# Kernel tuning notes

Hardware: AMD Instinct MI355X
Metric: run time of the kernel (lower is better)

## Reference

```python
import jax, jax.numpy as jnp
import numpy as np
from bisect import bisect

# hyperparameters (from init_kwargs)
DELTA = 1e-4
GAMMA = 0.1
UTILITY_SCALE = -0.01
PRIORITY_RAIL = 0.5
LOSS_BALANCE = 1.0
ALPHA_ELU = 1.0
ENTROPY_THRESHOLDS = [0, 10, 50]
ENTROPY_LEVELS = [0.0, 0.05, 0.1, 1.0]
MASK_LEVEL = 10000.0

N = 512


def setup_inputs() -> dict:
    key = jax.random.key(0)
    k1, k2, k3, k4 = jax.random.split(key, 4)
    soft_adj = jax.random.uniform(k1, (N, N), dtype=jnp.float32)
    # original adjacency is a binary {0,1} float mask
    original_adj = (jax.random.uniform(k2, (N, N)) > 0.5).astype(jnp.float32)
    distances = jax.random.uniform(k3, (N, N), dtype=jnp.float32) * 100.0
    flow = jax.random.uniform(k4, (N, N), dtype=jnp.float32) * 10.0
    epoch = 20  # python int, selects entropy penalty level via bisect
    return {"soft_adj": soft_adj, "original_adj": original_adj,
            "distances": distances, "flow": flow, "epoch": epoch}


def _shortest_path(soft_adj, distances):
    """Soft (softmin via logsumexp) Floyd-Warshall all-pairs shortest path."""
    W = distances / (soft_adj + DELTA)          # [N, N] effective edge weights
    n = W.shape[0]
    w0 = W * (1.0 - jnp.eye(n, dtype=W.dtype))  # zero diagonal

    def step(w, k):
        # softmin(w, w[:,k,None] + w[None,k,:]) without materializing a stack
        path_through_k = w[:, k][:, None] + w[k, :][None, :]
        w_new = -GAMMA * jnp.logaddexp(-w / GAMMA, -path_through_k / GAMMA)
        return w_new, None

    w_dist, _ = jax.lax.scan(step, w0, jnp.arange(n))
    return w_dist


def reference(soft_adj, original_adj, distances, flow, epoch):
    loss_cost = jnp.sum(soft_adj * distances)

    shortest_paths = _shortest_path(soft_adj, distances)

    exp_ut_rail = jnp.exp(UTILITY_SCALE * shortest_paths * PRIORITY_RAIL)
    exp_ut_base = jnp.exp(UTILITY_SCALE * distances)
    choice_matrix = exp_ut_rail / (exp_ut_rail + exp_ut_base)
    distance_saved = distances - PRIORITY_RAIL * shortest_paths
    utility_gain = flow * choice_matrix * distance_saved
    utility_gain = jax.nn.elu(utility_gain, alpha=ALPHA_ELU) + ALPHA_ELU

    inverse_soft = jnp.eye(soft_adj.shape[0], dtype=soft_adj.dtype) - soft_adj
    entropy_loss = jnp.sum(jnp.square(soft_adj * inverse_soft))
    entropy_scale = ENTROPY_LEVELS[bisect(ENTROPY_THRESHOLDS, epoch)]

    mask_loss = jnp.sum(soft_adj * (1.0 - original_adj))

    return (loss_cost
            + LOSS_BALANCE * jnp.sum(utility_gain)
            + entropy_loss * entropy_scale
            + MASK_LEVEL * mask_loss)
```

## Files before the change

kernel.cpp:

```cpp
#include <hip/hip_runtime.h>
#include <math.h>

#define NN 512
#define KP 64
#define NPANEL 8
#define NTHR 256
#define NBLK 256
#define TRUNITS (448 * 112)

#define D_   0
#define V_   4160
#define B2_  8320
#define UB_  12672
#define SB_  17024
#define H_   21376
#define LDSN 25728

__device__ __forceinline__ float einit(const float* s, const float* dI, int i, int j) {
  float w = dI[i * NN + j] / (s[i * NN + j] + 1e-4f);
  if (i == j) w = 0.f;
  return expf(-10.f * w);
}

__global__ __launch_bounds__(NTHR) void fw_phase(
    const float* __restrict__ s, const float* __restrict__ dI,
    float* __restrict__ E, float* __restrict__ Cs, float* __restrict__ Rs,
    float* __restrict__ out, int p) {
  __shared__ __align__(16) float lds[LDSN];
  const int blk = blockIdx.x, tid = threadIdx.x;
  const int k0 = p * KP;

  if (blk >= 32) {
    const int gt = (blk - 32) * NTHR + tid;
    if (p == 0) {
      if (blk == 32 && tid == 0) out[0] = 0.f;
      if (gt < TRUNITS) {
        const int ii = gt / 112;
        const int jj = gt - ii * 112;
        const int i = ii + KP;
        const int j = (jj + 16) << 2;
        const int idx = i * NN + j;
        const float4 sv = *(const float4*)(s + idx);
        const float4 dv = *(const float4*)(dI + idx);
        float w0 = dv.x / (sv.x + 1e-4f); if (i == j + 0) w0 = 0.f;
        float w1 = dv.y / (sv.y + 1e-4f); if (i == j + 1) w1 = 0.f;
        float w2 = dv.z / (sv.z + 1e-4f); if (i == j + 2) w2 = 0.f;
        float w3 = dv.w / (sv.w + 1e-4f); if (i == j + 3) w3 = 0.f;
        *(float4*)(E + idx) = make_float4(expf(-10.f * w0), expf(-10.f * w1),
                                          expf(-10.f * w2), expf(-10.f * w3));
      }
    } else if (gt < TRUNITS) {
      const int ii = gt / 112;
      const int jj = gt - ii * 112;
      const int i = (ii < k0) ? ii : ii + KP;
      const int j = ((jj < (p << 4)) ? jj : jj + 16) << 2;
      const int idx = i * NN + j;
      const float* Cprev = Cs + (size_t)(p - 1) * (NN * KP);
      const float* Rprev = Rs + (size_t)(p - 1) * (KP * NN);
      float4 acc = *(const float4*)(E + idx);
      const float* crow = Cprev + (size_t)i * KP;
      const float* rcol = Rprev + j;
#pragma unroll 8
      for (int r = 0; r < KP; ++r) {
        const float cv = crow[r];
        const float4 rv = *(const float4*)(rcol + (size_t)r * NN);
        acc.x += cv * rv.x; acc.y += cv * rv.y;
        acc.z += cv * rv.z; acc.w += cv * rv.w;
      }
      *(float4*)(E + idx) = acc;
    }
    return;
  }

  const bool isC = (blk < 16);
  const int sb = (blk >> 1) & 7;
  const int h = blk & 1;
  const int sOff = sb * KP;
  const bool haveSl = (sb != p);
  const float* Cprev = Cs + (size_t)(p - 1) * (NN * KP);
  const float* Rprev = Rs + (size_t)(p - 1) * (KP * NN);

  if (p == 0) {
    for (int e = tid; e < 4096; e += NTHR) {
      const int a = e >> 6, b = e & 63;
      const float v = einit(s, dI, a, b);
      lds[D_ + a * 65 + b] = v;
      if (blk == 0) E[a * NN + b] = v;
    }
    if (haveSl) {
      if (isC) {
        for (int e = tid; e < 2048; e += NTHR) {
          const int a = 32 * h + (e >> 6), b = e & 63;
          const float v = einit(s, dI, sOff + a, b);
          lds[V_ + a * 65 + b] = v;
          E[(sOff + a) * NN + b] = v;
        }
      } else {
        for (int e = tid; e < 2048; e += NTHR) {
          const int m = e >> 5, j = 32 * h + (e & 31);
          const float v = einit(s, dI, m, sOff + j);
          lds[V_ + j * 65 + m] = v;
          E[m * NN + (sOff + j)] = v;
        }
      }
    }
  } else {
#pragma unroll
    for (int k = 0; k < 4; ++k) {
      const int e4 = tid + k * NTHR;
      const int a = e4 >> 4, b4 = (e4 & 15) << 2;
      *(float4*)&lds[B2_ + a * 68 + b4] =
          *(const float4*)(Cprev + (size_t)(k0 + a) * KP + b4);
      *(float4*)&lds[UB_ + a * 68 + b4] =
          *(const float4*)(Rprev + (size_t)a * NN + (k0 + b4));
      if (haveSl) {
        if (isC)
          *(float4*)&lds[SB_ + a * 68 + b4] =
              *(const float4*)(Cprev + (size_t)(sOff + a) * KP + b4);
        else
          *(float4*)&lds[SB_ + a * 68 + b4] =
              *(const float4*)(Rprev + (size_t)a * NN + (sOff + b4));
      }
    }
    __syncthreads();
    {
      const int r0 = (tid >> 4) << 2, m0 = (tid & 15) << 2;
      float acc[4][4];
#pragma unroll
      for (int i2 = 0; i2 < 4; ++i2) {
        const float4 ev = *(const float4*)(E + (size_t)(k0 + r0 + i2) * NN + (k0 + m0));
        acc[i2][0] = ev.x; acc[i2][1] = ev.y; acc[i2][2] = ev.z; acc[i2][3] = ev.w;
      }
      for (int rr = 0; rr < KP; ++rr) {
        const float4 b4 = *(const float4*)&lds[UB_ + rr * 68 + m0];
#pragma unroll
        for (int i2 = 0; i2 < 4; ++i2) {
          const float av = lds[B2_ + (r0 + i2) * 68 + rr];
          acc[i2][0] += av * b4.x; acc[i2][1] += av * b4.y;
          acc[i2][2] += av * b4.z; acc[i2][3] += av * b4.w;
        }
      }
#pragma unroll
      for (int i2 = 0; i2 < 4; ++i2)
#pragma unroll
        for (int j2 = 0; j2 < 4; ++j2)
          lds[D_ + (r0 + i2) * 65 + (m0 + j2)] = acc[i2][j2];
    }
  }
  __syncthreads();

  if (tid < 64) {
    float x[64];
    if (isC) {
#pragma unroll
      for (int a = 0; a < 64; ++a) x[a] = lds[D_ + a * 65 + tid];
    } else {
#pragma unroll
      for (int a = 0; a < 64; ++a) x[a] = lds[D_ + tid * 65 + a];
    }
#pragma unroll
    for (int m = 0; m < 64; ++m) {
      const float xm = x[m];
      lds[H_ + m * 68 + tid] = xm;
#pragma unroll
      for (int a = 0; a < 64; ++a) {
        const int sa = __builtin_amdgcn_readlane(__float_as_int(x[a]), m);
        x[a] += __int_as_float(sa) * xm;
      }
    }
  } else if (tid < 192) {
    const int tt = tid - 64;
    if (haveSl && p > 0) {
      float acc[4][4];
      if (isC) {
        const int r0 = 32 * h + ((tt >> 4) << 2);
        const int m0 = (tt & 15) << 2;
#pragma unroll
        for (int i2 = 0; i2 < 4; ++i2) {
          const float4 ev = *(const float4*)(E + (size_t)(sOff + r0 + i2) * NN + (k0 + m0));
          acc[i2][0] = ev.x; acc[i2][1] = ev.y; acc[i2][2] = ev.z; acc[i2][3] = ev.w;
        }
        for (int rr = 0; rr < KP; ++rr) {
          const float4 b4 = *(const float4*)&lds[UB_ + rr * 68 + m0];
#pragma unroll
          for (int i2 = 0; i2 < 4; ++i2) {
            const float av = lds[SB_ + (r0 + i2) * 68 + rr];
            acc[i2][0] += av * b4.x; acc[i2][1] += av * b4.y;
            acc[i2][2] += av * b4.z; acc[i2][3] += av * b4.w;
          }
        }
#pragma unroll
        for (int i2 = 0; i2 < 4; ++i2) {
          *(float4*)(E + (size_t)(sOff + r0 + i2) * NN + (k0 + m0)) =
              make_float4(acc[i2][0], acc[i2][1], acc[i2][2], acc[i2][3]);
#pragma unroll
          for (int j2 = 0; j2 < 4; ++j2)
            lds[V_ + (r0 + i2) * 65 + (m0 + j2)] = acc[i2][j2];
        }
      } else {
        const int r0 = (tt & 15) << 2;
        const int c0 = 32 * h + ((tt >> 4) << 2);
#pragma unroll
        for (int i2 = 0; i2 < 4; ++i2) {
          const float4 ev = *(const float4*)(E + (size_t)(k0 + r0 + i2) * NN + (sOff + c0));
          acc[i2][0] = ev.x; acc[i2][1] = ev.y; acc[i2][2] = ev.z; acc[i2][3] = ev.w;
        }
        for (int rr = 0; rr < KP; ++rr) {
          const float4 b4 = *(const float4*)&lds[SB_ + rr * 68 + c0];
#pragma unroll
          for (int i2 = 0; i2 < 4; ++i2) {
            const float av = lds[B2_ + (r0 + i2) * 68 + rr];
            acc[i2][0] += av * b4.x; acc[i2][1] += av * b4.y;
            acc[i2][2] += av * b4.z; acc[i2][3] += av * b4.w;
          }
        }
#pragma unroll
        for (int i2 = 0; i2 < 4; ++i2) {
          *(float4*)(E + (size_t)(k0 + r0 + i2) * NN + (sOff + c0)) =
              make_float4(acc[i2][0], acc[i2][1], acc[i2][2], acc[i2][3]);
#pragma unroll
          for (int j2 = 0; j2 < 4; ++j2)
            lds[V_ + (c0 + j2) * 65 + (r0 + i2)] = acc[i2][j2];
        }
      }
    } else if (!haveSl) {
      for (int e = tt; e < 4096; e += 128) {
        const int a = e >> 6, b = e & 63;
        lds[V_ + a * 65 + b] = isC ? lds[D_ + a * 65 + b] : lds[D_ + b * 65 + a];
      }
    }
  }
  __syncthreads();

  for (int cch = 0; cch < 4; ++cch) {
    const int mb = cch * 16;
    if (cch > 0 && tid < 128) {
      const int r = 32 * h + (tid & 31);
      const int g = tid >> 5;
      const int m0c = mb + 4 * g;
      const int vb = V_ + r * 65;
      float a0 = lds[vb + m0c + 0], a1 = lds[vb + m0c + 1];
      float a2 = lds[vb + m0c + 2], a3 = lds[vb + m0c + 3];
      for (int mp = 0; mp < mb; ++mp) {
        const float vr = lds[vb + mp];
        const float4 u4 = *(const float4*)&lds[H_ + mp * 68 + m0c];
        a0 += vr * u4.x; a1 += vr * u4.y; a2 += vr * u4.z; a3 += vr * u4.w;
      }
      lds[vb + m0c + 0] = a0; lds[vb + m0c + 1] = a1;
      lds[vb + m0c + 2] = a2; lds[vb + m0c + 3] = a3;
    }
    __syncthreads();
    if (tid < 32) {
      const int r = 32 * h + tid;
      const int vb = V_ + r * 65 + mb;
      float v[16];
#pragma unroll
      for (int u2 = 0; u2 < 16; ++u2) v[u2] = lds[vb + u2];
#pragma unroll
      for (int mp = 0; mp < 15; ++mp) {
        const float vmp = v[mp];
#pragma unroll
        for (int m2 = mp + 1; m2 < 16; ++m2)
          v[m2] += vmp * lds[H_ + (mb + mp) * 68 + (mb + m2)];
      }
#pragma unroll
      for (int u2 = 0; u2 < 16; ++u2) lds[vb + u2] = v[u2];
    }
    __syncthreads();
  }

  float* Cp = Cs + (size_t)p * (NN * KP);
  float* Rp = Rs + (size_t)p * (KP * NN);
  if (isC) {
    for (int e = tid; e < 2048; e += NTHR) {
      const int a = 32 * h + (e >> 6), b = e & 63;
      Cp[(size_t)(sOff + a) * KP + b] = lds[V_ + a * 65 + b];
    }
  } else {
    for (int e = tid; e < 2048; e += NTHR) {
      const int m = e >> 5, j = 32 * h + (e & 31);
      Rp[(size_t)m * NN + (sOff + j)] = lds[V_ + j * 65 + m];
    }
  }
}

__device__ __forceinline__ float loss_elem(float Ev, float sv, float ov,
                                           float dv, float fv, int i, int j,
                                           float esc) {
  const float sp = (Ev > 0.f) ? (-0.1f * logf(Ev)) : 1e9f;
  const float ur = expf(-0.005f * sp);
  const float ub = expf(-0.01f * dv);
  const float choice = ur / (ur + ub);
  const float ug = fv * choice * (dv - 0.5f * sp);
  const float util = (ug > 0.f) ? (ug + 1.f) : expf(ug);
  const float ent = sv * (((i == j) ? 1.f : 0.f) - sv);
  return sv * dv + util + esc * ent * ent + 10000.f * (sv * (1.f - ov));
}

__global__ __launch_bounds__(NTHR) void k_loss(
    const float* __restrict__ s, const float* __restrict__ o,
    const float* __restrict__ dI, const float* __restrict__ f,
    const int* __restrict__ ep, const float* __restrict__ E,
    const float* __restrict__ Cs, const float* __restrict__ Rs,
    float* __restrict__ out) {
  __shared__ float red[NTHR];
  const int tid = threadIdx.x;
  const int g = blockIdx.x * NTHR + tid;
  const int idx0 = g * 4;
  const int i = idx0 >> 9;
  const int j = idx0 & (NN - 1);
  const float* C7 = Cs + (size_t)7 * (NN * KP);
  const float* R7 = Rs + (size_t)7 * (KP * NN);
  float4 acc = *(const float4*)(E + idx0);
  {
    const float* crow = C7 + (size_t)i * KP;
    const float* rcol = R7 + j;
#pragma unroll 8
    for (int r = 0; r < KP; ++r) {
      const float cv = crow[r];
      const float4 rv = *(const float4*)(rcol + (size_t)r * NN);
      acc.x += cv * rv.x; acc.y += cv * rv.y;
      acc.z += cv * rv.z; acc.w += cv * rv.w;
    }
  }
  const int bi = i >> 6, bj = j >> 6;
  if (bi == bj && bi >= 1) {
    const float* cf = Cs + (size_t)(bi - 1) * (NN * KP) + (size_t)i * KP;
    const float* rf = Rs + (size_t)(bi - 1) * (KP * NN) + j;
#pragma unroll 8
    for (int r = 0; r < KP; ++r) {
      const float cv = cf[r];
      const float4 rv = *(const float4*)(rf + (size_t)r * NN);
      acc.x += cv * rv.x; acc.y += cv * rv.y;
      acc.z += cv * rv.z; acc.w += cv * rv.w;
    }
  }
  const float4 sv = *(const float4*)(s + idx0);
  const float4 ov = *(const float4*)(o + idx0);
  const float4 dv = *(const float4*)(dI + idx0);
  const float4 fv = *(const float4*)(f + idx0);
  const int e = ep[0];
  const float esc = (e < 0) ? 0.f : (e < 10) ? 0.05f : (e < 50) ? 0.1f : 1.f;
  float lsum = loss_elem(acc.x, sv.x, ov.x, dv.x, fv.x, i, j + 0, esc)
             + loss_elem(acc.y, sv.y, ov.y, dv.y, fv.y, i, j + 1, esc)
             + loss_elem(acc.z, sv.z, ov.z, dv.z, fv.z, i, j + 2, esc)
             + loss_elem(acc.w, sv.w, ov.w, dv.w, fv.w, i, j + 3, esc);
  red[tid] = lsum;
  __syncthreads();
#pragma unroll
  for (int st = 128; st > 0; st >>= 1) {
    if (tid < st) red[tid] += red[tid + st];
    __syncthreads();
  }
  if (tid == 0) atomicAdd(out, red[0]);
}

extern "C" void kernel_launch(void* const* d_in, const int* in_sizes, int n_in,
                              void* d_out, int out_size, void* d_ws, size_t ws_size,
                              hipStream_t stream) {
  const float* s = (const float*)d_in[0];
  const float* o = (const float*)d_in[1];
  const float* d = (const float*)d_in[2];
  const float* f = (const float*)d_in[3];
  const int* ep = (const int*)d_in[4];

  float* E = (float*)d_ws;
  float* Cs = E + NN * NN;
  float* Rs = Cs + NPANEL * NN * KP;
  float* out = (float*)d_out;

  for (int p = 0; p < NPANEL; ++p)
    fw_phase<<<NBLK, NTHR, 0, stream>>>(s, d, E, Cs, Rs, out, p);
  k_loss<<<NBLK, NTHR, 0, stream>>>(s, o, d, f, ep, E, Cs, Rs, out);
}
```

Baseline: 244.5 us.

## Split panel-0 into a small kernel and fuse E initialization into phase one

Panel 0's pivot and panel factorization now run in a dedicated 32-block kernel that writes only the C and R panels. The initial exp-weight matrix is no longer materialized in E during phase 0; phase 1 computes those values on the fly from s and d wherever it would have read E. The diagonal block for phase 1 is written separately by otherwise idle threads. This removes a full pass of writing and re-reading E plus the wide phase-0 launch, at the cost of recomputing divisions and exps inside phase 1 and more branching.

```diff
diff --git a/kernel.cpp b/kernel.cpp
--- a/kernel.cpp
+++ b/kernel.cpp
@@ -22,53 +22,153 @@
   return expf(-10.f * w);
 }
 
+__global__ __launch_bounds__(NTHR) void fw_p0(
+    const float* __restrict__ s, const float* __restrict__ dI,
+    float* __restrict__ Cs, float* __restrict__ Rs, float* __restrict__ out) {
+  __shared__ __align__(16) float lds[LDSN];
+  const int blk = blockIdx.x, tid = threadIdx.x;
+  const bool isC = (blk < 16);
+  const int sb = (blk >> 1) & 7;
+  const int h = blk & 1;
+  const int sOff = sb * KP;
+  const bool haveSl = (sb != 0);
+  if (blk == 0 && tid == 0) out[0] = 0.f;
+
+  for (int e = tid; e < 4096; e += NTHR) {
+    const int a = e >> 6, b = e & 63;
+    lds[D_ + a * 65 + b] = einit(s, dI, a, b);
+  }
+  if (haveSl) {
+    if (isC) {
+      for (int e = tid; e < 2048; e += NTHR) {
+        const int a = 32 * h + (e >> 6), b = e & 63;
+        lds[V_ + a * 65 + b] = einit(s, dI, sOff + a, b);
+      }
+    } else {
+      for (int e = tid; e < 2048; e += NTHR) {
+        const int m = e >> 5, j = 32 * h + (e & 31);
+        lds[V_ + j * 65 + m] = einit(s, dI, m, sOff + j);
+      }
+    }
+  }
+  __syncthreads();
+
+  if (tid < 64) {
+    float x[64];
+    if (isC) {
+#pragma unroll
+      for (int a = 0; a < 64; ++a) x[a] = lds[D_ + a * 65 + tid];
+    } else {
+#pragma unroll
+      for (int a = 0; a < 64; ++a) x[a] = lds[D_ + tid * 65 + a];
+    }
+#pragma unroll
+    for (int m = 0; m < 64; ++m) {
+      const float xm = x[m];
+      lds[H_ + m * 68 + tid] = xm;
+#pragma unroll
+      for (int a = 0; a < 64; ++a) {
+        const int sa = __builtin_amdgcn_readlane(__float_as_int(x[a]), m);
+        x[a] += __int_as_float(sa) * xm;
+      }
+    }
+  } else if (tid < 192) {
+    if (!haveSl) {
+      for (int e = tid - 64; e < 4096; e += 128) {
+        const int a = e >> 6, b = e & 63;
+        lds[V_ + a * 65 + b] = isC ? lds[D_ + a * 65 + b] : lds[D_ + b * 65 + a];
+      }
+    }
+  }
+  __syncthreads();
+
+  for (int cch = 0; cch < 4; ++cch) {
+    const int mb = cch * 16;
+    if (cch > 0 && tid < 128) {
+      const int r = 32 * h + (tid & 31);
+      const int g = tid >> 5;
+      const int m0c = mb + 4 * g;
+      const int vb = V_ + r * 65;
+      float a0 = lds[vb + m0c + 0], a1 = lds[vb + m0c + 1];
+      float a2 = lds[vb + m0c + 2], a3 = lds[vb + m0c + 3];
+      for (int mp = 0; mp < mb; ++mp) {
+        const float vr = lds[vb + mp];
+        const float4 u4 = *(const float4*)&lds[H_ + mp * 68 + m0c];
+        a0 += vr * u4.x; a1 += vr * u4.y; a2 += vr * u4.z; a3 += vr * u4.w;
+      }
+      lds[vb + m0c + 0] = a0; lds[vb + m0c + 1] = a1;
+      lds[vb + m0c + 2] = a2; lds[vb + m0c + 3] = a3;
+    }
+    __syncthreads();
+    if (tid < 32) {
+      const int r = 32 * h + tid;
+      const int vb = V_ + r * 65 + mb;
+      float v[16];
+#pragma unroll
+      for (int u2 = 0; u2 < 16; ++u2) v[u2] = lds[vb + u2];
+#pragma unroll
+      for (int mp = 0; mp < 15; ++mp) {
+        const float vmp = v[mp];
+#pragma unroll
+        for (int m2 = mp + 1; m2 < 16; ++m2)
+          v[m2] += vmp * lds[H_ + (mb + mp) * 68 + (mb + m2)];
+      }
+#pragma unroll
+      for (int u2 = 0; u2 < 16; ++u2) lds[vb + u2] = v[u2];
+    }
+    __syncthreads();
+  }
+
+  if (isC) {
+    for (int e = tid; e < 2048; e += NTHR) {
+      const int a = 32 * h + (e >> 6), b = e & 63;
+      Cs[(size_t)(sOff + a) * KP + b] = lds[V_ + a * 65 + b];
+    }
+  } else {
+    for (int e = tid; e < 2048; e += NTHR) {
+      const int m = e >> 5, j = 32 * h + (e & 31);
+      Rs[(size_t)m * NN + (sOff + j)] = lds[V_ + j * 65 + m];
+    }
+  }
+}
+
 __global__ __launch_bounds__(NTHR) void fw_phase(
     const float* __restrict__ s, const float* __restrict__ dI,
     float* __restrict__ E, float* __restrict__ Cs, float* __restrict__ Rs,
-    float* __restrict__ out, int p) {
+    int p) {
   __shared__ __align__(16) float lds[LDSN];
   const int blk = blockIdx.x, tid = threadIdx.x;
   const int k0 = p * KP;
+  const float* Cprev = Cs + (size_t)(p - 1) * (NN * KP);
+  const float* Rprev = Rs + (size_t)(p - 1) * (KP * NN);
 
   if (blk >= 32) {
     const int gt = (blk - 32) * NTHR + tid;
-    if (p == 0) {
-      if (blk == 32 && tid == 0) out[0] = 0.f;
-      if (gt < TRUNITS) {
-        const int ii = gt / 112;
-        const int jj = gt - ii * 112;
-        const int i = ii + KP;
-        const int j = (jj + 16) << 2;
-        const int idx = i * NN + j;
-        const float4 sv = *(const float4*)(s + idx);
-        const float4 dv = *(const float4*)(dI + idx);
-        float w0 = dv.x / (sv.x + 1e-4f); if (i == j + 0) w0 = 0.f;
-        float w1 = dv.y / (sv.y + 1e-4f); if (i == j + 1) w1 = 0.f;
-        float w2 = dv.z / (sv.z + 1e-4f); if (i == j + 2) w2 = 0.f;
-        float w3 = dv.w / (sv.w + 1e-4f); if (i == j + 3) w3 = 0.f;
-        *(float4*)(E + idx) = make_float4(expf(-10.f * w0), expf(-10.f * w1),
-                                          expf(-10.f * w2), expf(-10.f * w3));
-      }
-    } else if (gt < TRUNITS) {
-      const int ii = gt / 112;
-      const int jj = gt - ii * 112;
-      const int i = (ii < k0) ? ii : ii + KP;
-      const int j = ((jj < (p << 4)) ? jj : jj + 16) << 2;
-      const int idx = i * NN + j;
-      const float* Cprev = Cs + (size_t)(p - 1) * (NN * KP);
-      const float* Rprev = Rs + (size_t)(p - 1) * (KP * NN);
-      float4 acc = *(const float4*)(E + idx);
-      const float* crow = Cprev + (size_t)i * KP;
-      const float* rcol = Rprev + j;
+    if (gt >= TRUNITS) return;
+    const int ii = gt / 112;
+    const int jj = gt - ii * 112;
+    const int i = (ii < k0) ? ii : ii + KP;
+    const int j = ((jj < (p << 4)) ? jj : jj + 16) << 2;
+    const int idx = i * NN + j;
+    float4 acc;
+    if (p == 1) {
+      acc.x = einit(s, dI, i, j + 0);
+      acc.y = einit(s, dI, i, j + 1);
+      acc.z = einit(s, dI, i, j + 2);
+      acc.w = einit(s, dI, i, j + 3);
+    } else {
+      acc = *(const float4*)(E + idx);
+    }
+    const float* crow = Cprev + (size_t)i * KP;
+    const float* rcol = Rprev + j;
 #pragma unroll 8
-      for (int r = 0; r < KP; ++r) {
-        const float cv = crow[r];
-        const float4 rv = *(const float4*)(rcol + (size_t)r * NN);
-        acc.x += cv * rv.x; acc.y += cv * rv.y;
-        acc.z += cv * rv.z; acc.w += cv * rv.w;
-      }
-      *(float4*)(E + idx) = acc;
-    }
+    for (int r = 0; r < KP; ++r) {
+      const float cv = crow[r];
+      const float4 rv = *(const float4*)(rcol + (size_t)r * NN);
+      acc.x += cv * rv.x; acc.y += cv * rv.y;
+      acc.z += cv * rv.z; acc.w += cv * rv.w;
+    }
+    *(float4*)(E + idx) = acc;
     return;
   }
 
@@ -77,75 +177,63 @@
   const int h = blk & 1;
   const int sOff = sb * KP;
   const bool haveSl = (sb != p);
-  const float* Cprev = Cs + (size_t)(p - 1) * (NN * KP);
-  const float* Rprev = Rs + (size_t)(p - 1) * (KP * NN);
-
-  if (p == 0) {
-    for (int e = tid; e < 4096; e += NTHR) {
-      const int a = e >> 6, b = e & 63;
-      const float v = einit(s, dI, a, b);
-      lds[D_ + a * 65 + b] = v;
-      if (blk == 0) E[a * NN + b] = v;
-    }
+
+  const int r0d = (tid >> 4) << 2, m0d = (tid & 15) << 2;
+  float4 epre[4];
+  if (p == 1) {
+#pragma unroll
+    for (int i2 = 0; i2 < 4; ++i2) {
+      epre[i2].x = einit(s, dI, k0 + r0d + i2, k0 + m0d + 0);
+      epre[i2].y = einit(s, dI, k0 + r0d + i2, k0 + m0d + 1);
+      epre[i2].z = einit(s, dI, k0 + r0d + i2, k0 + m0d + 2);
+      epre[i2].w = einit(s, dI, k0 + r0d + i2, k0 + m0d + 3);
+    }
+  } else {
+#pragma unroll
+    for (int i2 = 0; i2 < 4; ++i2)
+      epre[i2] = *(const float4*)(E + (size_t)(k0 + r0d + i2) * NN + (k0 + m0d));
+  }
+
+#pragma unroll
+  for (int k = 0; k < 4; ++k) {
+    const int e4 = tid + k * NTHR;
+    const int a = e4 >> 4, b4 = (e4 & 15) << 2;
+    *(float4*)&lds[B2_ + a * 68 + b4] =
+        *(const float4*)(Cprev + (size_t)(k0 + a) * KP + b4);
+    *(float4*)&lds[UB_ + a * 68 + b4] =
+        *(const float4*)(Rprev + (size_t)a * NN + (k0 + b4));
     if (haveSl) {
-      if (isC) {
-        for (int e = tid; e < 2048; e += NTHR) {
-          const int a = 32 * h + (e >> 6), b = e & 63;
-          const float v = einit(s, dI, sOff + a, b);
-          lds[V_ + a * 65 + b] = v;
-          E[(sOff + a) * NN + b] = v;
-        }
-      } else {
-        for (int e = tid; e < 2048; e += NTHR) {
-          const int m = e >> 5, j = 32 * h + (e & 31);
-          const float v = einit(s, dI, m, sOff + j);
-          lds[V_ + j * 65 + m] = v;
-          E[m * NN + (sOff + j)] = v;
-        }
-      }
-    }
-  } else {
-#pragma unroll
-    for (int k = 0; k < 4; ++k) {
-      const int e4 = tid + k * NTHR;
-      const int a = e4 >> 4, b4 = (e4 & 15) << 2;
-      *(float4*)&lds[B2_ + a * 68 + b4] =
-          *(const float4*)(Cprev + (size_t)(k0 + a) * KP + b4);
-      *(float4*)&lds[UB_ + a * 68 + b4] =
-          *(const float4*)(Rprev + (size_t)a * NN + (k0 + b4));
-      if (haveSl) {
-        if (isC)
-          *(float4*)&lds[SB_ + a * 68 + b4] =
-              *(const float4*)(Cprev + (size_t)(sOff + a) * KP + b4);
-        else
-          *(float4*)&lds[SB_ + a * 68 + b4] =
-              *(const float4*)(Rprev + (size_t)a * NN + (sOff + b4));
-      }
-    }
-    __syncthreads();
-    {
-      const int r0 = (tid >> 4) << 2, m0 = (tid & 15) << 2;
-      float acc[4][4];
+      if (isC)
+        *(float4*)&lds[SB_ + a * 68 + b4] =
+            *(const float4*)(Cprev + (size_t)(sOff + a) * KP + b4);
+      else
+        *(float4*)&lds[SB_ + a * 68 + b4] =
+            *(const float4*)(Rprev + (size_t)a * NN + (sOff + b4));
+    }
+  }
+  __syncthreads();
+
+  {
+    float acc[4][4];
+#pragma unroll
+    for (int i2 = 0; i2 < 4; ++i2) {
+      acc[i2][0] = epre[i2].x; acc[i2][1] = epre[i2].y;
+      acc[i2][2] = epre[i2].z; acc[i2][3] = epre[i2].w;
+    }
+    for (int rr = 0; rr < KP; ++rr) {
+      const float4 b4 = *(const float4*)&lds[UB_ + rr * 68 + m0d];
 #pragma unroll
       for (int i2 = 0; i2 < 4; ++i2) {
-        const float4 ev = *(const float4*)(E + (size_t)(k0 + r0 + i2) * NN + (k0 + m0));
-        acc[i2][0] = ev.x; acc[i2][1] = ev.y; acc[i2][2] = ev.z; acc[i2][3] = ev.w;
-      }
-      for (int rr = 0; rr < KP; ++rr) {
-        const float4 b4 = *(const float4*)&lds[UB_ + rr * 68 + m0];
-#pragma unroll
-        for (int i2 = 0; i2 < 4; ++i2) {
-          const float av = lds[B2_ + (r0 + i2) * 68 + rr];
-          acc[i2][0] += av * b4.x; acc[i2][1] += av * b4.y;
-          acc[i2][2] += av * b4.z; acc[i2][3] += av * b4.w;
-        }
-      }
-#pragma unroll
-      for (int i2 = 0; i2 < 4; ++i2)
-#pragma unroll
-        for (int j2 = 0; j2 < 4; ++j2)
-          lds[D_ + (r0 + i2) * 65 + (m0 + j2)] = acc[i2][j2];
-    }
+        const float av = lds[B2_ + (r0d + i2) * 68 + rr];
+        acc[i2][0] += av * b4.x; acc[i2][1] += av * b4.y;
+        acc[i2][2] += av * b4.z; acc[i2][3] += av * b4.w;
+      }
+    }
+#pragma unroll
+    for (int i2 = 0; i2 < 4; ++i2)
+#pragma unroll
+      for (int j2 = 0; j2 < 4; ++j2)
+        lds[D_ + (r0d + i2) * 65 + (m0d + j2)] = acc[i2][j2];
   }
   __syncthreads();
 
@@ -170,15 +258,25 @@
     }
   } else if (tid < 192) {
     const int tt = tid - 64;
-    if (haveSl && p > 0) {
+    if (haveSl) {
       float acc[4][4];
       if (isC) {
         const int r0 = 32 * h + ((tt >> 4) << 2);
         const int m0 = (tt & 15) << 2;
-#pragma unroll
-        for (int i2 = 0; i2 < 4; ++i2) {
-          const float4 ev = *(const float4*)(E + (size_t)(sOff + r0 + i2) * NN + (k0 + m0));
-          acc[i2][0] = ev.x; acc[i2][1] = ev.y; acc[i2][2] = ev.z; acc[i2][3] = ev.w;
+        if (p == 1) {
+#pragma unroll
+          for (int i2 = 0; i2 < 4; ++i2) {
+            acc[i2][0] = einit(s, dI, sOff + r0 + i2, k0 + m0 + 0);
+            acc[i2][1] = einit(s, dI, sOff + r0 + i2, k0 + m0 + 1);
+            acc[i2][2] = einit(s, dI, sOff + r0 + i2, k0 + m0 + 2);
+            acc[i2][3] = einit(s, dI, sOff + r0 + i2, k0 + m0 + 3);
+          }
+        } else {
+#pragma unroll
+          for (int i2 = 0; i2 < 4; ++i2) {
+            const float4 ev = *(const float4*)(E + (size_t)(sOff + r0 + i2) * NN + (k0 + m0));
+            acc[i2][0] = ev.x; acc[i2][1] = ev.y; acc[i2][2] = ev.z; acc[i2][3] = ev.w;
+          }
         }
         for (int rr = 0; rr < KP; ++rr) {
           const float4 b4 = *(const float4*)&lds[UB_ + rr * 68 + m0];
@@ -200,10 +298,20 @@
       } else {
         const int r0 = (tt & 15) << 2;
         const int c0 = 32 * h + ((tt >> 4) << 2);
-#pragma unroll
-        for (int i2 = 0; i2 < 4; ++i2) {
-          const float4 ev = *(const float4*)(E + (size_t)(k0 + r0 + i2) * NN + (sOff + c0));
-          acc[i2][0] = ev.x; acc[i2][1] = ev.y; acc[i2][2] = ev.z; acc[i2][3] = ev.w;
+        if (p == 1) {
+#pragma unroll
+          for (int i2 = 0; i2 < 4; ++i2) {
+            acc[i2][0] = einit(s, dI, k0 + r0 + i2, sOff + c0 + 0);
+            acc[i2][1] = einit(s, dI, k0 + r0 + i2, sOff + c0 + 1);
+            acc[i2][2] = einit(s, dI, k0 + r0 + i2, sOff + c0 + 2);
+            acc[i2][3] = einit(s, dI, k0 + r0 + i2, sOff + c0 + 3);
+          }
+        } else {
+#pragma unroll
+          for (int i2 = 0; i2 < 4; ++i2) {
+            const float4 ev = *(const float4*)(E + (size_t)(k0 + r0 + i2) * NN + (sOff + c0));
+            acc[i2][0] = ev.x; acc[i2][1] = ev.y; acc[i2][2] = ev.z; acc[i2][3] = ev.w;
+          }
         }
         for (int rr = 0; rr < KP; ++rr) {
           const float4 b4 = *(const float4*)&lds[SB_ + rr * 68 + c0];
@@ -223,10 +331,17 @@
             lds[V_ + (c0 + j2) * 65 + (r0 + i2)] = acc[i2][j2];
         }
       }
-    } else if (!haveSl) {
+    } else {
       for (int e = tt; e < 4096; e += 128) {
         const int a = e >> 6, b = e & 63;
         lds[V_ + a * 65 + b] = isC ? lds[D_ + a * 65 + b] : lds[D_ + b * 65 + a];
+      }
+    }
+  } else {
+    if (p == 1 && !haveSl && isC) {
+      for (int e = 2048 * h + (tid - 192); e < 2048 * (h + 1); e += 64) {
+        const int a = e >> 6, b = e & 63;
+        E[(size_t)(k0 + a) * NN + (k0 + b)] = einit(s, dI, k0 + a, k0 + b);
       }
     }
   }
@@ -369,7 +484,8 @@
   float* Rs = Cs + NPANEL * NN * KP;
   float* out = (float*)d_out;
 
-  for (int p = 0; p < NPANEL; ++p)
-    fw_phase<<<NBLK, NTHR, 0, stream>>>(s, d, E, Cs, Rs, out, p);
+  fw_p0<<<32, NTHR, 0, stream>>>(s, d, Cs, Rs, out);
+  for (int p = 1; p < NPANEL; ++p)
+    fw_phase<<<NBLK, NTHR, 0, stream>>>(s, d, E, Cs, Rs, p);
   k_loss<<<NBLK, NTHR, 0, stream>>>(s, o, d, f, ep, E, Cs, Rs, out);
 }
```

New measurement: 246.8 us. Within noise of the previous version (+0.9%).
